# Kernel tuning notes

Hardware: AMD Instinct MI355X
Metric: run time of the kernel (lower is better)

The kernel has to match this reference:

```python
import jax, jax.numpy as jnp
import numpy as np

D_MODEL = 2048
N_HEADS = 16
HEAD_DIM = 128
ROPE_THETA = 10000.0


def _rope_cache(seq_len, dim, theta):
    inv_freq = 1.0 / (theta ** (jnp.arange(0, dim, 2, dtype=jnp.float32) / dim))
    t = jnp.arange(seq_len, dtype=jnp.float32)
    freqs = jnp.outer(t, inv_freq)          # [T, dim/2]
    emb = jnp.concatenate([freqs, freqs], axis=-1)  # [T, dim]
    return jnp.cos(emb), jnp.sin(emb)


def _rotate_half(x):
    d = x.shape[-1] // 2
    return jnp.concatenate([-x[..., d:], x[..., :d]], axis=-1)


def setup_inputs() -> dict:
    key = jax.random.key(0)
    k1, k2, k3 = jax.random.split(key, 3)
    B, T, D = 2, 2048, D_MODEL
    x = jax.random.normal(k1, (B, T, D), dtype=jnp.float32)
    w_qkv = jax.random.normal(k2, (D, 3 * D), dtype=jnp.float32) * (D ** -0.5)
    w_out = jax.random.normal(k3, (D, D), dtype=jnp.float32) * (D ** -0.5)
    return {"x": x, "w_qkv": w_qkv, "w_out": w_out}


def reference(x, w_qkv, w_out):
    B, T, D = x.shape
    H, Hd = N_HEADS, HEAD_DIM
    qkv = x @ w_qkv                                  # [B, T, 3D]
    q, k, v = jnp.split(qkv, 3, axis=-1)
    # [B, H, T, Hd]
    q = q.reshape(B, T, H, Hd).transpose(0, 2, 1, 3)
    k = k.reshape(B, T, H, Hd).transpose(0, 2, 1, 3)
    v = v.reshape(B, T, H, Hd).transpose(0, 2, 1, 3)
    cos, sin = _rope_cache(T, Hd, ROPE_THETA)        # [T, Hd]
    cos = cos[None, None]                            # [1,1,T,Hd]
    sin = sin[None, None]
    q = q * cos + _rotate_half(q) * sin
    k = k * cos + _rotate_half(k) * sin
    scale = Hd ** -0.5
    logits = jnp.einsum('bhqd,bhkd->bhqk', q, k) * scale
    causal = jnp.tril(jnp.ones((T, T), dtype=bool))
    logits = jnp.where(causal[None, None], logits, jnp.finfo(logits.dtype).min)
    attn = jax.nn.softmax(logits, axis=-1)
    out = jnp.einsum('bhqk,bhkd->bhqd', attn, v)     # [B,H,T,Hd]
    out = out.transpose(0, 2, 1, 3).reshape(B, T, D)
    return out @ w_out
```

## Files before the change

### kernel.cpp

```cpp
#include <hip/hip_runtime.h>

typedef unsigned short u16;
typedef unsigned int u32;
typedef __bf16 bf16x8 __attribute__((ext_vector_type(8)));
typedef float f32x4 __attribute__((ext_vector_type(4)));
typedef u16 u16x4 __attribute__((ext_vector_type(4)));
typedef u16 u16x8 __attribute__((ext_vector_type(8)));

#define T_SEQ 2048
#define DMODEL 2048
#define NQKV 6144
#define HD 128
#define NH 16
#define MROWS 4096

__device__ __forceinline__ u16 f2b(float f) {
  union { float f; u32 u; } a; a.f = f;
  u32 r = a.u + 0x7fffu + ((a.u >> 16) & 1u);
  return (u16)(r >> 16);
}
__device__ __forceinline__ float b2f(u16 h) {
  union { u32 u; float f; } a; a.u = ((u32)h) << 16;
  return a.f;
}
__device__ __forceinline__ void g2l16(const u16* g, u16* l) {
  __builtin_amdgcn_global_load_lds((const __attribute__((address_space(1))) u32*)g,
                                   (__attribute__((address_space(3))) u32*)l, 16, 0, 0);
}

__global__ void k_f32_to_bf16(const float* __restrict__ in, u16* __restrict__ out, int n) {
  int i = (blockIdx.x * 256 + threadIdx.x) * 8;
  if (i >= n) return;
  float4 a = *(const float4*)(in + i);
  float4 b = *(const float4*)(in + i + 4);
  u16x8 v;
  v[0] = f2b(a.x); v[1] = f2b(a.y); v[2] = f2b(a.z); v[3] = f2b(a.w);
  v[4] = f2b(b.x); v[5] = f2b(b.y); v[6] = f2b(b.z); v[7] = f2b(b.w);
  *(u16x8*)(out + i) = v;
}

__global__ void k_transpose_bf16(const float* __restrict__ in, u16* __restrict__ out,
                                 int R, int C) {
  __shared__ u16 tile[32][33];
  const int c0 = blockIdx.x * 32, r0 = blockIdx.y * 32;
  const int tx = threadIdx.x & 31, ty = threadIdx.x >> 5;
#pragma unroll
  for (int i = 0; i < 32; i += 8)
    tile[ty + i][tx] = f2b(in[(size_t)(r0 + ty + i) * C + c0 + tx]);
  __syncthreads();
#pragma unroll
  for (int i = 0; i < 32; i += 8)
    out[(size_t)(c0 + ty + i) * R + r0 + tx] = tile[tx][ty + i];
}

__global__ __launch_bounds__(256) void k_gemm_qkv(const u16* __restrict__ A,
                                                  const u16* __restrict__ B,
                                                  u16* __restrict__ qr,
                                                  u16* __restrict__ kr,
                                                  u16* __restrict__ vtb) {
  __shared__ __align__(16) u16 lA[128 * 64];
  __shared__ __align__(16) u16 lB[128 * 64];
  const int K = DMODEL;
  const int tid = threadIdx.x;
  const int wid = tid >> 6, lane = tid & 63;
  const int g = lane >> 4, q = lane & 15;
  const int wr = wid >> 1, wc = wid & 1;
  const int bn = blockIdx.x, bm = blockIdx.y;
  const int l8 = lane >> 3, l7 = lane & 7;
  const f32x4 fzero = {0.f, 0.f, 0.f, 0.f};
  f32x4 acc[4][4];
#pragma unroll
  for (int m = 0; m < 4; ++m)
#pragma unroll
    for (int n = 0; n < 4; ++n) acc[m][n] = fzero;

  const u16* Ab = A + (size_t)bm * 128 * K;
  const u16* Bb = B + (size_t)bn * 128 * K;

  for (int k0 = 0; k0 < K; k0 += 64) {
    __syncthreads();
#pragma unroll
    for (int i = 0; i < 4; ++i) {
      int chunk = wid * 4 + i;
      int row = chunk * 8 + l8;
      int scol = (l7 * 8) ^ ((row & 7) << 3);
      g2l16(Ab + (size_t)row * K + k0 + scol, lA + chunk * 512);
      g2l16(Bb + (size_t)row * K + k0 + scol, lB + chunk * 512);
    }
    __syncthreads();
#pragma unroll
    for (int kk = 0; kk < 2; ++kk) {
      bf16x8 af[4], bfr[4];
#pragma unroll
      for (int m = 0; m < 4; ++m) {
        int row = wr * 64 + m * 16 + q;
        int col = (kk * 32 + g * 8) ^ ((row & 7) << 3);
        af[m] = *(const bf16x8*)(lA + row * 64 + col);
      }
#pragma unroll
      for (int n = 0; n < 4; ++n) {
        int row = wc * 32 + (n & 1) * 16 + (n >> 1) * 64 + q;
        int col = (kk * 32 + g * 8) ^ ((row & 7) << 3);
        bfr[n] = *(const bf16x8*)(lB + row * 64 + col);
      }
#pragma unroll
      for (int m = 0; m < 4; ++m)
#pragma unroll
        for (int n = 0; n < 4; ++n)
          acc[m][n] = __builtin_amdgcn_mfma_f32_16x16x32_bf16(af[m], bfr[n], acc[m][n], 0, 0, 0);
    }
  }
  __builtin_amdgcn_sched_barrier(0);

  const int h = bn & 15;
  const int which = bn >> 4;
  const int b = bm >> 4;
  const int bh = b * 16 + h;
  const int tb0 = (bm & 15) * 128 + wr * 64;
  const float qscale = 0.08838834764831845f;

  if (which == 2) {
    u16* vdst = vtb + (size_t)bh * HD * T_SEQ;
#pragma unroll
    for (int m = 0; m < 4; ++m)
#pragma unroll
      for (int n = 0; n < 4; ++n) {
        int c = wc * 32 + (n & 1) * 16 + (n >> 1) * 64 + q;
        int t0 = tb0 + m * 16 + g * 4;
        u16x4 pk;
#pragma unroll
        for (int r = 0; r < 4; ++r) pk[r] = f2b(acc[m][n][r]);
        *(u16x4*)(vdst + (size_t)c * T_SEQ + t0) = pk;
      }
  } else {
    u16* dst = (which ? kr : qr) + (size_t)bh * T_SEQ * HD;
    const float sc = which ? 1.0f : qscale;
#pragma unroll
    for (int n = 0; n < 2; ++n) {
      int dm = wc * 32 + n * 16 + q;
      float inv = exp2f(-(float)dm * 0.20762050592046521f);
#pragma unroll
      for (int m = 0; m < 4; ++m)
#pragma unroll
        for (int r = 0; r < 4; ++r) {
          int t = tb0 + m * 16 + g * 4 + r;
          float s, c;
          __sincosf((float)t * inv, &s, &c);
          float x0 = acc[m][n][r];
          float x1 = acc[m][n + 2][r];
          u32 pk = (u32)f2b((x0 * c - x1 * s) * sc) |
                   ((u32)f2b((x1 * c + x0 * s) * sc) << 16);
          *(u32*)(dst + (size_t)t * HD + dm * 2) = pk;
        }
    }
  }
}

template <int EPI>
__global__ __launch_bounds__(256) void k_gemm_nt(const u16* __restrict__ A,
                                                 const u16* __restrict__ B,
                                                 void* __restrict__ Cv,
                                                 int M, int N, int K) {
  __shared__ __align__(16) u16 lA[128 * 64];
  __shared__ __align__(16) u16 lB[128 * 64];
  const int tid = threadIdx.x;
  const int wid = tid >> 6, lane = tid & 63;
  const int g = lane >> 4, q = lane & 15;
  const int wr = wid >> 1, wc = wid & 1;
  const int bn = blockIdx.x, bm = blockIdx.y;
  const int l8 = lane >> 3, l7 = lane & 7;
  const f32x4 fzero = {0.f, 0.f, 0.f, 0.f};
  f32x4 acc[4][4];
#pragma unroll
  for (int m = 0; m < 4; ++m)
#pragma unroll
    for (int n = 0; n < 4; ++n) acc[m][n] = fzero;

  const u16* Ab = A + (size_t)bm * 128 * K;
  const u16* Bb = B + (size_t)bn * 128 * K;

  for (int k0 = 0; k0 < K; k0 += 64) {
    __syncthreads();
#pragma unroll
    for (int i = 0; i < 4; ++i) {
      int chunk = wid * 4 + i;
      int row = chunk * 8 + l8;
      int scol = (l7 * 8) ^ ((row & 7) << 3);
      g2l16(Ab + (size_t)row * K + k0 + scol, lA + chunk * 512);
      g2l16(Bb + (size_t)row * K + k0 + scol, lB + chunk * 512);
    }
    __syncthreads();
#pragma unroll
    for (int kk = 0; kk < 2; ++kk) {
      bf16x8 af[4], bfr[4];
#pragma unroll
      for (int m = 0; m < 4; ++m) {
        int row = wr * 64 + m * 16 + q;
        int col = (kk * 32 + g * 8) ^ ((row & 7) << 3);
        af[m] = *(const bf16x8*)(lA + row * 64 + col);
      }
#pragma unroll
      for (int n = 0; n < 4; ++n) {
        int row = wc * 64 + n * 16 + q;
        int col = (kk * 32 + g * 8) ^ ((row & 7) << 3);
        bfr[n] = *(const bf16x8*)(lB + row * 64 + col);
      }
#pragma unroll
      for (int m = 0; m < 4; ++m)
#pragma unroll
        for (int n = 0; n < 4; ++n)
          acc[m][n] = __builtin_amdgcn_mfma_f32_16x16x32_bf16(af[m], bfr[n], acc[m][n], 0, 0, 0);
    }
  }
  const int rbase = bm * 128 + wr * 64;
  const int cbase = bn * 128 + wc * 64;
#pragma unroll
  for (int m = 0; m < 4; ++m)
#pragma unroll
    for (int n = 0; n < 4; ++n) {
      int col = cbase + n * 16 + q;
#pragma unroll
      for (int r = 0; r < 4; ++r) {
        int row = rbase + m * 16 + g * 4 + r;
        if (EPI == 0)
          ((u16*)Cv)[(size_t)row * N + col] = f2b(acc[m][n][r]);
        else
          ((float*)Cv)[(size_t)row * N + col] = acc[m][n][r];
      }
    }
}

__global__ __launch_bounds__(256) void k_attn(const u16* __restrict__ qr,
                                              const u16* __restrict__ kr,
                                              const u16* __restrict__ vtb,
                                              u16* __restrict__ ao) {
  __shared__ __align__(16) u16 lK[2][64 * 128];
  __shared__ __align__(16) u16 lV[2][128 * 64];
  __shared__ __align__(16) u16 lP[4][16 * 72];
  const int bh = blockIdx.x, b = bh >> 4, h = bh & 15;
  const int tid = threadIdx.x;
  const int wid = tid >> 6, lane = tid & 63;
  const int g = lane >> 4, q = lane & 15;
  const int l8 = lane >> 3, l7 = lane & 7;
  const u16* qb = qr + (size_t)bh * T_SEQ * HD;
  const u16* kbp = kr + (size_t)bh * T_SEQ * HD;
  const u16* vb = vtb + (size_t)bh * HD * T_SEQ;
  const f32x4 fzero = {0.f, 0.f, 0.f, 0.f};

  auto stageKV = [&](int kb, int bufI) {
#pragma unroll
    for (int i = 0; i < 4; ++i) {
      int chunk = wid * 4 + i;
      int row = chunk * 4 + g;
      int scol = (q * 8) ^ ((row & 7) << 3);
      g2l16(kbp + (size_t)(kb + row) * HD + scol, &lK[bufI][chunk * 512]);
    }
#pragma unroll
    for (int i = 0; i < 4; ++i) {
      int chunk = wid * 4 + i;
      int row = chunk * 8 + l8;
      int scol = (l7 * 8) ^ ((row & 7) << 3);
      g2l16(vb + (size_t)row * T_SEQ + kb + scol, &lV[bufI][chunk * 512]);
    }
  };

  for (int half = 0; half < 2; ++half) {
    const int qt = half ? (int)blockIdx.y : 31 - (int)blockIdx.y;
    const int qw0 = qt * 64 + wid * 16;

    bf16x8 qf[4];
#pragma unroll
    for (int ks = 0; ks < 4; ++ks)
      qf[ks] = *(const bf16x8*)(qb + (size_t)(qw0 + q) * HD + ks * 32 + g * 8);

    f32x4 o_acc[8];
#pragma unroll
    for (int n = 0; n < 8; ++n) o_acc[n] = fzero;
    float m_run = -1e30f, l_run = 0.f;

    const int ntiles = qt + 1;
    stageKV(0, 0);
    __syncthreads();
    for (int kt = 0; kt < ntiles; ++kt) {
      const int kb = kt * 64;
      const int cb = kt & 1;
      if (kt + 1 < ntiles) stageKV(kb + 64, cb ^ 1);
      const u16* lKc = lK[cb];
      const u16* lVc = lV[cb];
      {
        f32x4 st[4];
#pragma unroll
        for (int m = 0; m < 4; ++m) st[m] = fzero;
#pragma unroll
        for (int ks = 0; ks < 4; ++ks) {
#pragma unroll
          for (int m = 0; m < 4; ++m) {
            int row = m * 16 + q;
            int col = (ks * 32 + g * 8) ^ ((row & 7) << 3);
            bf16x8 kf = *(const bf16x8*)(lKc + row * 128 + col);
            st[m] = __builtin_amdgcn_mfma_f32_16x16x32_bf16(kf, qf[ks], st[m], 0, 0, 0);
          }
        }
        const int qrow = qw0 + q;
        float p[4][4];
        float pmax = -1e30f;
        if (kt == ntiles - 1) {
#pragma unroll
          for (int m = 0; m < 4; ++m)
#pragma unroll
            for (int r = 0; r < 4; ++r) {
              int kcol = kb + m * 16 + g * 4 + r;
              float s = (kcol <= qrow) ? st[m][r] : -1e30f;
              p[m][r] = s;
              pmax = fmaxf(pmax, s);
            }
        } else {
#pragma unroll
          for (int m = 0; m < 4; ++m)
#pragma unroll
            for (int r = 0; r < 4; ++r) {
              p[m][r] = st[m][r];
              pmax = fmaxf(pmax, st[m][r]);
            }
        }
        pmax = fmaxf(pmax, __shfl_xor(pmax, 16));
        pmax = fmaxf(pmax, __shfl_xor(pmax, 32));
        float m_new = fmaxf(m_run, pmax);
        float corr = __expf(m_run - m_new);
        float ls = 0.f;
#pragma unroll
        for (int m = 0; m < 4; ++m)
#pragma unroll
          for (int r = 0; r < 4; ++r) {
            float e = __expf(p[m][r] - m_new);
            p[m][r] = e;
            ls += e;
          }
        ls += __shfl_xor(ls, 16);
        ls += __shfl_xor(ls, 32);
        l_run = l_run * corr + ls;
        m_run = m_new;
#pragma unroll
        for (int m = 0; m < 4; ++m) {
#pragma unroll
          for (int rp = 0; rp < 2; ++rp) {
            u32 pk = (u32)f2b(p[m][rp * 2]) | ((u32)f2b(p[m][rp * 2 + 1]) << 16);
            *(u32*)(&lP[wid][q * 72 + m * 16 + g * 4 + rp * 2]) = pk;
          }
        }
        asm volatile("s_waitcnt lgkmcnt(0)" ::: "memory");
        __builtin_amdgcn_sched_barrier(0);
        float corr4[4];
#pragma unroll
        for (int r = 0; r < 4; ++r) corr4[r] = __shfl(corr, g * 4 + r);
#pragma unroll
        for (int n = 0; n < 8; ++n) {
#pragma unroll
          for (int r = 0; r < 4; ++r) o_acc[n][r] *= corr4[r];
        }
#pragma unroll
        for (int ks = 0; ks < 2; ++ks) {
          bf16x8 pf = *(const bf16x8*)(&lP[wid][q * 72 + ks * 32 + g * 8]);
#pragma unroll
          for (int n = 0; n < 8; ++n) {
            int row = n * 16 + q;
            int col = (ks * 32 + g * 8) ^ ((row & 7) << 3);
            bf16x8 vf = *(const bf16x8*)(lVc + row * 64 + col);
            o_acc[n] = __builtin_amdgcn_mfma_f32_16x16x32_bf16(pf, vf, o_acc[n], 0, 0, 0);
          }
        }
      }
      __syncthreads();
    }
    float linv[4];
#pragma unroll
    for (int r = 0; r < 4; ++r) {
      float lv = __shfl(l_run, g * 4 + r);
      linv[r] = 1.0f / lv;
    }
#pragma unroll
    for (int n = 0; n < 8; ++n)
#pragma unroll
      for (int r = 0; r < 4; ++r) {
        int trow = qw0 + g * 4 + r;
        ao[(size_t)(b * T_SEQ + trow) * DMODEL + h * HD + n * 16 + q] = f2b(o_acc[n][r] * linv[r]);
      }
  }
}

extern "C" void kernel_launch(void* const* d_in, const int* in_sizes, int n_in,
                              void* d_out, int out_size, void* d_ws, size_t ws_size,
                              hipStream_t stream) {
  const float* x = (const float*)d_in[0];
  const float* w_qkv = (const float*)d_in[1];
  const float* w_out = (const float*)d_in[2];
  char* ws = (char*)d_ws;
  size_t off = 0;
  u16* xb = (u16*)(ws + off);    off += (size_t)MROWS * DMODEL * 2;
  u16* wqkvT = (u16*)(ws + off); off += (size_t)NQKV * DMODEL * 2;
  u16* woutT = (u16*)(ws + off); off += (size_t)DMODEL * DMODEL * 2;
  u16* qr = (u16*)(ws + off);    off += (size_t)32 * T_SEQ * HD * 2;
  u16* kr = (u16*)(ws + off);    off += (size_t)32 * T_SEQ * HD * 2;
  u16* vtb = (u16*)(ws + off);   off += (size_t)32 * T_SEQ * HD * 2;
  u16* ao = xb;

  k_f32_to_bf16<<<dim3(MROWS * DMODEL / (256 * 8)), 256, 0, stream>>>(x, xb, MROWS * DMODEL);
  k_transpose_bf16<<<dim3(NQKV / 32, DMODEL / 32), 256, 0, stream>>>(w_qkv, wqkvT, DMODEL, NQKV);
  k_transpose_bf16<<<dim3(DMODEL / 32, DMODEL / 32), 256, 0, stream>>>(w_out, woutT, DMODEL, DMODEL);
  k_gemm_qkv<<<dim3(48, 32), 256, 0, stream>>>(xb, wqkvT, qr, kr, vtb);
  k_attn<<<dim3(32, 16), 256, 0, stream>>>(qr, kr, vtb, ao);
  k_gemm_nt<1><<<dim3(DMODEL / 128, MROWS / 128), 256, 0, stream>>>(ao, woutT, d_out, MROWS, DMODEL, DMODEL);
}
```

Measured before the change: 263.9 us.

## Stage QKV epilogue through LDS for coalesced stores; skip unneeded softmax rescale

The QKV GEMM epilogue now writes accumulators into the freed shared-memory tiles and reads them back so that RoPE rotation and V-transpose stores run on contiguous, coalesced rows, instead of scattered per-lane writes. The rotary frequency is computed once per lane. The attention loop also skips the output rescale and exp correction when no row maximum grows within the wave. The cost is extra LDS round trips and barriers in the epilogue, plus a wave vote and a branch in the softmax loop.

Result: slower. 269.4 us (+2.1%).

```diff
diff --git a/kernel.cpp b/kernel.cpp
--- a/kernel.cpp
+++ b/kernel.cpp
@@ -58,8 +58,10 @@
                                                   u16* __restrict__ qr,
                                                   u16* __restrict__ kr,
                                                   u16* __restrict__ vtb) {
-  __shared__ __align__(16) u16 lA[128 * 64];
-  __shared__ __align__(16) u16 lB[128 * 64];
+  __shared__ __align__(16) u16 lsmem[2][128 * 64];
+  u16* lA = lsmem[0];
+  u16* lB = lsmem[1];
+  float* ldsF = (float*)lsmem;
   const int K = DMODEL;
   const int tid = threadIdx.x;
   const int wid = tid >> 6, lane = tid & 63;
@@ -116,42 +118,57 @@
   const int which = bn >> 4;
   const int b = bm >> 4;
   const int bh = b * 16 + h;
-  const int tb0 = (bm & 15) * 128 + wr * 64;
-  const float qscale = 0.08838834764831845f;
-
-  if (which == 2) {
-    u16* vdst = vtb + (size_t)bh * HD * T_SEQ;
-#pragma unroll
-    for (int m = 0; m < 4; ++m)
+  const int tbase = (bm & 15) * 128;
+  const float sc = (which == 0) ? 0.08838834764831845f : 1.0f;
+  u16* dst = (which ? kr : qr) + (size_t)bh * T_SEQ * HD;
+  u16* vdst = vtb + (size_t)bh * HD * T_SEQ;
+  const float inv = exp2f(-(float)lane * 0.20762050592046521f);
+
+#pragma unroll
+  for (int p = 0; p < 2; ++p) {
+    __syncthreads();
+#pragma unroll
+    for (int mm = 0; mm < 2; ++mm) {
 #pragma unroll
       for (int n = 0; n < 4; ++n) {
         int c = wc * 32 + (n & 1) * 16 + (n >> 1) * 64 + q;
-        int t0 = tb0 + m * 16 + g * 4;
+#pragma unroll
+        for (int r = 0; r < 4; ++r) {
+          int lr = wr * 32 + mm * 16 + g * 4 + r;
+          ldsF[lr * 128 + (c ^ ((lr & 7) << 2))] = acc[2 * p + mm][n][r];
+        }
+      }
+    }
+    __syncthreads();
+    if (which == 2) {
+#pragma unroll 2
+      for (int j = 0; j < 8; ++j) {
+        int d = j * 16 + (tid >> 4);
+        int tq = tid & 15;
+        int lr0 = tq * 4;
         u16x4 pk;
 #pragma unroll
-        for (int r = 0; r < 4; ++r) pk[r] = f2b(acc[m][n][r]);
-        *(u16x4*)(vdst + (size_t)c * T_SEQ + t0) = pk;
-      }
-  } else {
-    u16* dst = (which ? kr : qr) + (size_t)bh * T_SEQ * HD;
-    const float sc = which ? 1.0f : qscale;
-#pragma unroll
-    for (int n = 0; n < 2; ++n) {
-      int dm = wc * 32 + n * 16 + q;
-      float inv = exp2f(-(float)dm * 0.20762050592046521f);
-#pragma unroll
-      for (int m = 0; m < 4; ++m)
-#pragma unroll
-        for (int r = 0; r < 4; ++r) {
-          int t = tb0 + m * 16 + g * 4 + r;
-          float s, c;
-          __sincosf((float)t * inv, &s, &c);
-          float x0 = acc[m][n][r];
-          float x1 = acc[m][n + 2][r];
-          u32 pk = (u32)f2b((x0 * c - x1 * s) * sc) |
-                   ((u32)f2b((x1 * c + x0 * s) * sc) << 16);
-          *(u32*)(dst + (size_t)t * HD + dm * 2) = pk;
-        }
+        for (int rr = 0; rr < 4; ++rr) {
+          int lr = lr0 + rr;
+          pk[rr] = f2b(ldsF[lr * 128 + (d ^ ((lr & 7) << 2))]);
+        }
+        int t0 = tbase + (lr0 >> 5) * 64 + p * 32 + (lr0 & 31);
+        *(u16x4*)(vdst + (size_t)d * T_SEQ + t0) = pk;
+      }
+    } else {
+#pragma unroll 2
+      for (int j = 0; j < 16; ++j) {
+        int row = wid * 16 + j;
+        int xk = (row & 7) << 2;
+        float x0 = ldsF[row * 128 + (lane ^ xk)];
+        float x1 = ldsF[row * 128 + ((lane + 64) ^ xk)];
+        int t = tbase + (row >> 5) * 64 + p * 32 + (row & 31);
+        float s, c;
+        __sincosf((float)t * inv, &s, &c);
+        u32 pk = (u32)f2b((x0 * c - x1 * s) * sc) |
+                 ((u32)f2b((x1 * c + x0 * s) * sc) << 16);
+        *(u32*)(dst + (size_t)t * HD + lane * 2) = pk;
+      }
     }
   }
 }
@@ -325,8 +342,8 @@
         }
         pmax = fmaxf(pmax, __shfl_xor(pmax, 16));
         pmax = fmaxf(pmax, __shfl_xor(pmax, 32));
-        float m_new = fmaxf(m_run, pmax);
-        float corr = __expf(m_run - m_new);
+        const bool noresc = __all(pmax <= m_run);
+        const float m_new = noresc ? m_run : fmaxf(m_run, pmax);
         float ls = 0.f;
 #pragma unroll
         for (int m = 0; m < 4; ++m)
@@ -338,8 +355,6 @@
           }
         ls += __shfl_xor(ls, 16);
         ls += __shfl_xor(ls, 32);
-        l_run = l_run * corr + ls;
-        m_run = m_new;
 #pragma unroll
         for (int m = 0; m < 4; ++m) {
 #pragma unroll
@@ -350,13 +365,20 @@
         }
         asm volatile("s_waitcnt lgkmcnt(0)" ::: "memory");
         __builtin_amdgcn_sched_barrier(0);
-        float corr4[4];
-#pragma unroll
-        for (int r = 0; r < 4; ++r) corr4[r] = __shfl(corr, g * 4 + r);
-#pragma unroll
-        for (int n = 0; n < 8; ++n) {
-#pragma unroll
-          for (int r = 0; r < 4; ++r) o_acc[n][r] *= corr4[r];
+        if (noresc) {
+          l_run += ls;
+        } else {
+          float corr = __expf(m_run - m_new);
+          l_run = l_run * corr + ls;
+          m_run = m_new;
+          float corr4[4];
+#pragma unroll
+          for (int r = 0; r < 4; ++r) corr4[r] = __shfl(corr, g * 4 + r);
+#pragma unroll
+          for (int n = 0; n < 8; ++n) {
+#pragma unroll
+            for (int r = 0; r < 4; ++r) o_acc[n][r] *= corr4[r];
+          }
         }
 #pragma unroll
         for (int ks = 0; ks < 2; ++ks) {
```
